# Kernel tuning notes

Hardware: AMD Instinct MI355X
Metric: run time of the kernel (lower is better)

The kernel has to match this reference:

```python
import jax, jax.numpy as jnp
import numpy as np

B, S, D, H = 4, 2048, 1024, 16
DK = D // H

def setup_inputs() -> dict:
    key = jax.random.key(0)
    ks = jax.random.split(key, 9)
    s = 1.0 / np.sqrt(D)
    return {
        "x":  jax.random.normal(ks[0], (B, S, D), dtype=jnp.float32),
        "Wq": jax.random.uniform(ks[1], (D, D), jnp.float32, -s, s),
        "bq": jax.random.uniform(ks[2], (D,), jnp.float32, -s, s),
        "Wk": jax.random.uniform(ks[3], (D, D), jnp.float32, -s, s),
        "bk": jax.random.uniform(ks[4], (D,), jnp.float32, -s, s),
        "Wv": jax.random.uniform(ks[5], (D, D), jnp.float32, -s, s),
        "bv": jax.random.uniform(ks[6], (D,), jnp.float32, -s, s),
        "Wo": jax.random.uniform(ks[7], (D, D), jnp.float32, -s, s),
        "bo": jax.random.uniform(ks[8], (D,), jnp.float32, -s, s),
    }

def reference(x, Wq, bq, Wk, bk, Wv, bv, Wo, bo):
    # Q/K/V projections: [B,S,D] -> [B,H,S,DK]
    def proj(W, b):
        return (x @ W.T + b).reshape(B, S, H, DK).transpose(0, 2, 1, 3)
    Q, K, V = proj(Wq, bq), proj(Wk, bk), proj(Wv, bv)
    scale = 1.0 / np.sqrt(DK).astype(np.float32)
    scores = jnp.einsum('bhqd,bhkd->bhqk', Q, K) * scale  # [B,H,S,S]
    attn = jax.nn.softmax(scores, axis=-1)                 # dropout = identity (eval)
    out = jnp.einsum('bhqk,bhkd->bhqd', attn, V)           # [B,H,S,DK]
    out = out.transpose(0, 2, 1, 3).reshape(B, S, D)
    return out @ Wo.T + bo, attn
```

## Files before the change

### kernel.cpp

```cpp
#include <hip/hip_runtime.h>
#include <hip/hip_bf16.h>

#define Bb 4
#define Ss 2048
#define Dd 1024
#define Hh 16
#define DKk 64

typedef float f32x4 __attribute__((ext_vector_type(4)));
typedef short bf16x8 __attribute__((ext_vector_type(8)));

#define MFMA16(a, b, c) __builtin_amdgcn_mfma_f32_16x16x32_bf16((a), (b), (c), 0, 0, 0)

__device__ __forceinline__ unsigned short f2bf(float f) {
  union { float f; unsigned u; } v;
  v.f = f;
  unsigned r = v.u + 0x7FFFu + ((v.u >> 16) & 1u);
  return (unsigned short)(r >> 16);
}

__device__ __forceinline__ float fast_exp2(float x) {
  float r;
  asm("v_exp_f32 %0, %1" : "=v"(r) : "v"(x));
  return r;
}

__device__ __forceinline__ bf16x8 cvt8(float4 f0, float4 f1) {
  bf16x8 r;
  r[0] = (short)f2bf(f0.x); r[1] = (short)f2bf(f0.y);
  r[2] = (short)f2bf(f0.z); r[3] = (short)f2bf(f0.w);
  r[4] = (short)f2bf(f1.x); r[5] = (short)f2bf(f1.y);
  r[6] = (short)f2bf(f1.z); r[7] = (short)f2bf(f1.w);
  return r;
}

__global__ __launch_bounds__(256) void qkv_proj_kernel(
    const float* __restrict__ X,
    const float* __restrict__ Wq, const float* __restrict__ bq,
    const float* __restrict__ Wk, const float* __restrict__ bk_,
    const float* __restrict__ Wv, const float* __restrict__ bv_,
    unsigned short* __restrict__ qo, unsigned short* __restrict__ ko,
    unsigned short* __restrict__ vo)
{
  __shared__ unsigned short Al[128][72];
  __shared__ unsigned short Bl[128][72];
  const int tid = threadIdx.x;
  const int lane = tid & 63, wid = tid >> 6;
  const int m0 = blockIdx.x * 128;
  const int sel = blockIdx.y >> 3;
  const int n0 = (blockIdx.y & 7) * 128;
  const float* W; const float* bias; unsigned short* out; float prescale;
  if (sel == 0)      { W = Wq; bias = bq;  out = qo; prescale = 0.125f; }
  else if (sel == 1) { W = Wk; bias = bk_; out = ko; prescale = 1.0f;  }
  else               { W = Wv; bias = bv_; out = vo; prescale = 1.0f;  }

  const int wm = (wid >> 1) * 64, wn = (wid & 1) * 64;
  const int lr = lane & 15, lk8 = (lane >> 4) * 8;

  f32x4 acc[4][4] = {};

  for (int k0 = 0; k0 < Dd; k0 += 64) {
#pragma unroll
    for (int it = 0; it < 4; ++it) {
      int idx = it * 256 + tid;
      int row = idx >> 3;
      int ch = (idx & 7) * 8;
      const float* pa = X + (size_t)(m0 + row) * Dd + k0 + ch;
      const float* pb = W + (size_t)(n0 + row) * Dd + k0 + ch;
      float4 a0 = *(const float4*)pa;
      float4 a1 = *(const float4*)(pa + 4);
      float4 b0 = *(const float4*)pb;
      float4 b1 = *(const float4*)(pb + 4);
      *(bf16x8*)&Al[row][ch] = cvt8(a0, a1);
      *(bf16x8*)&Bl[row][ch] = cvt8(b0, b1);
    }
    __syncthreads();
#pragma unroll
    for (int ks = 0; ks < 2; ++ks) {
      const int kk = ks * 32 + lk8;
      bf16x8 av[4], bv[4];
#pragma unroll
      for (int i = 0; i < 4; ++i)
        av[i] = *(const bf16x8*)&Al[wm + i * 16 + lr][kk];
#pragma unroll
      for (int j = 0; j < 4; ++j)
        bv[j] = *(const bf16x8*)&Bl[wn + j * 16 + lr][kk];
#pragma unroll
      for (int i = 0; i < 4; ++i)
#pragma unroll
        for (int j = 0; j < 4; ++j)
          acc[i][j] = MFMA16(av[i], bv[j], acc[i][j]);
    }
    __syncthreads();
  }

  const int rg = (lane >> 4) * 4;
#pragma unroll
  for (int i = 0; i < 4; ++i) {
#pragma unroll
    for (int j = 0; j < 4; ++j) {
      int n = n0 + wn + j * 16 + lr;
      float bvv = bias[n];
      int hh = n >> 6, dk = n & 63;
#pragma unroll
      for (int r = 0; r < 4; ++r) {
        int m = m0 + wm + i * 16 + rg + r;
        int bb = m >> 11, ss = m & (Ss - 1);
        float v = (acc[i][j][r] + bvv) * prescale;
        out[((size_t)(bb * Hh + hh) * Ss + ss) * DKk + dk] = f2bf(v);
      }
    }
  }
}

__global__ __launch_bounds__(256) void attn_kernel(
    const unsigned short* __restrict__ Qw, const unsigned short* __restrict__ Kw,
    const unsigned short* __restrict__ Vw, float* __restrict__ attn,
    unsigned short* __restrict__ OH)
{
  __shared__ unsigned short VT[64][72];
  __shared__ unsigned short Pl[4][32][72];
  const int tid = threadIdx.x, lane = tid & 63, wid = tid >> 6;
  const int bh = blockIdx.y;
  const int q0 = blockIdx.x * 128 + wid * 32;
  const unsigned short* Qh = Qw + (size_t)bh * Ss * DKk;
  const unsigned short* Kh = Kw + (size_t)bh * Ss * DKk;
  const unsigned short* Vh = Vw + (size_t)bh * Ss * DKk;
  const int lr = lane & 15;
  const int lk8 = (lane >> 4) * 8;
  const int rg = (lane >> 4) * 4;
  const float L2E = 1.44269504088896f;

  bf16x8 aq[2][2];
#pragma unroll
  for (int mi = 0; mi < 2; ++mi)
#pragma unroll
    for (int ks = 0; ks < 2; ++ks)
      aq[mi][ks] = *(const bf16x8*)&Qh[(size_t)(q0 + mi * 16 + lr) * DKk + ks * 32 + lk8];

  float lsum[2] = {0.f, 0.f};
  for (int kb = 0; kb < Ss; kb += 64) {
    bf16x8 bk[4][2];
#pragma unroll
    for (int nj = 0; nj < 4; ++nj)
#pragma unroll
      for (int ks = 0; ks < 2; ++ks)
        bk[nj][ks] = *(const bf16x8*)&Kh[(size_t)(kb + nj * 16 + lr) * DKk + ks * 32 + lk8];
#pragma unroll
    for (int mi = 0; mi < 2; ++mi) {
      float acc = 0.f;
#pragma unroll
      for (int nj = 0; nj < 4; ++nj) {
        f32x4 c = {};
        c = MFMA16(bk[nj][0], aq[mi][0], c);
        c = MFMA16(bk[nj][1], aq[mi][1], c);
        acc += fast_exp2(c[0] * L2E) + fast_exp2(c[1] * L2E) +
               fast_exp2(c[2] * L2E) + fast_exp2(c[3] * L2E);
      }
      lsum[mi] += acc;
    }
  }
  float linv[2];
#pragma unroll
  for (int mi = 0; mi < 2; ++mi) {
    float l = lsum[mi];
    l += __shfl_xor(l, 16, 64);
    l += __shfl_xor(l, 32, 64);
    linv[mi] = 1.0f / l;
  }

  f32x4 o[2][4] = {};
  float* attn_bh = attn + (size_t)bh * Ss * Ss;
  for (int kb = 0; kb < Ss; kb += 64) {
    __syncthreads();
    {
      int key = tid >> 2;
      int d0 = (tid & 3) * 16;
      bf16x8 v0 = *(const bf16x8*)&Vh[(size_t)(kb + key) * DKk + d0];
      bf16x8 v1 = *(const bf16x8*)&Vh[(size_t)(kb + key) * DKk + d0 + 8];
#pragma unroll
      for (int i = 0; i < 8; ++i) VT[d0 + i][key] = (unsigned short)v0[i];
#pragma unroll
      for (int i = 0; i < 8; ++i) VT[d0 + 8 + i][key] = (unsigned short)v1[i];
    }
    __syncthreads();

    bf16x8 bk[4][2];
#pragma unroll
    for (int nj = 0; nj < 4; ++nj)
#pragma unroll
      for (int ks = 0; ks < 2; ++ks)
        bk[nj][ks] = *(const bf16x8*)&Kh[(size_t)(kb + nj * 16 + lr) * DKk + ks * 32 + lk8];

#pragma unroll
    for (int mi = 0; mi < 2; ++mi) {
      const int q = q0 + mi * 16 + lr;
      const float li = linv[mi];
      float* arow = attn_bh + (size_t)q * Ss + kb;
#pragma unroll
      for (int nj = 0; nj < 4; ++nj) {
        f32x4 c = {};
        c = MFMA16(bk[nj][0], aq[mi][0], c);
        c = MFMA16(bk[nj][1], aq[mi][1], c);
        float p0 = fast_exp2(c[0] * L2E) * li;
        float p1 = fast_exp2(c[1] * L2E) * li;
        float p2 = fast_exp2(c[2] * L2E) * li;
        float p3 = fast_exp2(c[3] * L2E) * li;
        f32x4 pv4 = {p0, p1, p2, p3};
        __builtin_nontemporal_store(pv4, (f32x4*)(arow + nj * 16 + rg));
        unsigned w0 = (unsigned)f2bf(p0) | ((unsigned)f2bf(p1) << 16);
        unsigned w1 = (unsigned)f2bf(p2) | ((unsigned)f2bf(p3) << 16);
        uint2 w = {w0, w1};
        *(uint2*)&Pl[wid][mi * 16 + lr][nj * 16 + rg] = w;
      }
    }
#pragma unroll
    for (int ks = 0; ks < 2; ++ks) {
      const int kk = ks * 32 + lk8;
      bf16x8 ap[2], bv[4];
#pragma unroll
      for (int mi = 0; mi < 2; ++mi)
        ap[mi] = *(const bf16x8*)&Pl[wid][mi * 16 + lr][kk];
#pragma unroll
      for (int nj = 0; nj < 4; ++nj)
        bv[nj] = *(const bf16x8*)&VT[nj * 16 + lr][kk];
#pragma unroll
      for (int mi = 0; mi < 2; ++mi)
#pragma unroll
        for (int nj = 0; nj < 4; ++nj)
          o[mi][nj] = MFMA16(ap[mi], bv[nj], o[mi][nj]);
    }
  }

  const int b = bh >> 4, h = bh & 15;
#pragma unroll
  for (int mi = 0; mi < 2; ++mi)
#pragma unroll
    for (int nj = 0; nj < 4; ++nj)
#pragma unroll
      for (int r = 0; r < 4; ++r) {
        int q = q0 + mi * 16 + rg + r;
        int d = nj * 16 + lr;
        OH[(((size_t)b * Ss + q) * Hh + h) * DKk + d] = f2bf(o[mi][nj][r]);
      }
}

__global__ __launch_bounds__(256) void oproj_kernel(
    const unsigned short* __restrict__ A, const float* __restrict__ W,
    const float* __restrict__ bias, float* __restrict__ out)
{
  __shared__ unsigned short Al[128][72];
  __shared__ unsigned short Bl[128][72];
  const int tid = threadIdx.x;
  const int lane = tid & 63, wid = tid >> 6;
  const int m0 = blockIdx.x * 128;
  const int n0 = blockIdx.y * 128;
  const int wm = (wid >> 1) * 64, wn = (wid & 1) * 64;
  const int lr = lane & 15, lk8 = (lane >> 4) * 8;

  f32x4 acc[4][4] = {};

  for (int k0 = 0; k0 < Dd; k0 += 64) {
#pragma unroll
    for (int it = 0; it < 4; ++it) {
      int idx = it * 256 + tid;
      int row = idx >> 3;
      int ch = (idx & 7) * 8;
      *(bf16x8*)&Al[row][ch] = *(const bf16x8*)&A[(size_t)(m0 + row) * Dd + k0 + ch];
      const float* pb = W + (size_t)(n0 + row) * Dd + k0 + ch;
      float4 b0 = *(const float4*)pb;
      float4 b1 = *(const float4*)(pb + 4);
      *(bf16x8*)&Bl[row][ch] = cvt8(b0, b1);
    }
    __syncthreads();
#pragma unroll
    for (int ks = 0; ks < 2; ++ks) {
      const int kk = ks * 32 + lk8;
      bf16x8 av[4], bv[4];
#pragma unroll
      for (int i = 0; i < 4; ++i)
        av[i] = *(const bf16x8*)&Al[wm + i * 16 + lr][kk];
#pragma unroll
      for (int j = 0; j < 4; ++j)
        bv[j] = *(const bf16x8*)&Bl[wn + j * 16 + lr][kk];
#pragma unroll
      for (int i = 0; i < 4; ++i)
#pragma unroll
        for (int j = 0; j < 4; ++j)
          acc[i][j] = MFMA16(av[i], bv[j], acc[i][j]);
    }
    __syncthreads();
  }

  const int rg = (lane >> 4) * 4;
#pragma unroll
  for (int i = 0; i < 4; ++i) {
#pragma unroll
    for (int j = 0; j < 4; ++j) {
      int n = n0 + wn + j * 16 + lr;
      float bvv = bias[n];
#pragma unroll
      for (int r = 0; r < 4; ++r) {
        int m = m0 + wm + i * 16 + rg + r;
        out[(size_t)m * Dd + n] = acc[i][j][r] + bvv;
      }
    }
  }
}

extern "C" void kernel_launch(void* const* d_in, const int* in_sizes, int n_in,
                              void* d_out, int out_size, void* d_ws, size_t ws_size,
                              hipStream_t stream) {
  const float* x  = (const float*)d_in[0];
  const float* Wq = (const float*)d_in[1];
  const float* bq = (const float*)d_in[2];
  const float* Wk = (const float*)d_in[3];
  const float* bk = (const float*)d_in[4];
  const float* Wv = (const float*)d_in[5];
  const float* bv = (const float*)d_in[6];
  const float* Wo = (const float*)d_in[7];
  const float* bo = (const float*)d_in[8];

  float* out  = (float*)d_out;
  float* attn = out + (size_t)Bb * Ss * Dd;

  const size_t headElems = (size_t)Bb * Hh * Ss * DKk;
  unsigned short* qws = (unsigned short*)d_ws;
  unsigned short* kws = qws + headElems;
  unsigned short* vws = kws + headElems;
  unsigned short* ohw = vws + headElems;

  dim3 blk(256);
  qkv_proj_kernel<<<dim3(64, 24), blk, 0, stream>>>(x, Wq, bq, Wk, bk, Wv, bv,
                                                    qws, kws, vws);
  attn_kernel<<<dim3(16, 64), blk, 0, stream>>>(qws, kws, vws, attn, ohw);
  oproj_kernel<<<dim3(64, 8), blk, 0, stream>>>(ohw, Wo, bo, out);
}
```

Measured before the change: 620.5 us.

## Pre-cast inputs to bf16, use direct global-to-LDS loads, write V transposed

Adds a cast kernel that converts x and all weight matrices to bf16 once, so the GEMM kernels can stage tiles with global_load_lds instead of per-thread fp32 loads and conversions. The QKV kernel now writes V in a transposed [bh][dk][s] layout, which lets the attention kernel read V fragments straight from global memory and drop the LDS transpose and two barriers per key block. The attention grid is also remapped to a 1D index that groups heads. The cost is an extra launch plus a round trip through global memory for the bf16 copies, and the GEMM LDS tiles lose their padding, which may cause bank conflicts.

```diff
diff --git a/kernel.cpp b/kernel.cpp
--- a/kernel.cpp
+++ b/kernel.cpp
@@ -9,6 +9,7 @@
 
 typedef float f32x4 __attribute__((ext_vector_type(4)));
 typedef short bf16x8 __attribute__((ext_vector_type(8)));
+typedef unsigned short u16x4 __attribute__((ext_vector_type(4)));
 
 #define MFMA16(a, b, c) __builtin_amdgcn_mfma_f32_16x16x32_bf16((a), (b), (c), 0, 0, 0)
 
@@ -34,57 +35,82 @@
   return r;
 }
 
-__global__ __launch_bounds__(256) void qkv_proj_kernel(
-    const float* __restrict__ X,
-    const float* __restrict__ Wq, const float* __restrict__ bq,
-    const float* __restrict__ Wk, const float* __restrict__ bk_,
-    const float* __restrict__ Wv, const float* __restrict__ bv_,
+__global__ __launch_bounds__(256) void cast_all(
+    const float* __restrict__ x,  const float* __restrict__ Wq,
+    const float* __restrict__ Wk, const float* __restrict__ Wv,
+    const float* __restrict__ Wo,
+    unsigned short* __restrict__ xb,  unsigned short* __restrict__ wqb,
+    unsigned short* __restrict__ wkb, unsigned short* __restrict__ wvb,
+    unsigned short* __restrict__ wob)
+{
+  int bid = blockIdx.x;
+  const float* s; unsigned short* d; size_t base8;
+  if (bid < 4096) { s = x; d = xb; base8 = (size_t)bid * 256; }
+  else {
+    int t = bid - 4096; int w = t >> 9; int off = t & 511;
+    s = (w == 0) ? Wq : (w == 1) ? Wk : (w == 2) ? Wv : Wo;
+    d = (w == 0) ? wqb : (w == 1) ? wkb : (w == 2) ? wvb : wob;
+    base8 = (size_t)off * 256;
+  }
+  size_t i8 = base8 + threadIdx.x;
+  const float4* sp = (const float4*)s + 2 * i8;
+  float4 a = sp[0], b = sp[1];
+  *(bf16x8*)(d + i8 * 8) = cvt8(a, b);
+}
+
+__global__ __launch_bounds__(256) void qkv_kernel(
+    const unsigned short* __restrict__ xb,
+    const unsigned short* __restrict__ wqb, const float* __restrict__ bq,
+    const unsigned short* __restrict__ wkb, const float* __restrict__ bk_,
+    const unsigned short* __restrict__ wvb, const float* __restrict__ bv_,
     unsigned short* __restrict__ qo, unsigned short* __restrict__ ko,
-    unsigned short* __restrict__ vo)
+    unsigned short* __restrict__ vto)
 {
-  __shared__ unsigned short Al[128][72];
-  __shared__ unsigned short Bl[128][72];
-  const int tid = threadIdx.x;
-  const int lane = tid & 63, wid = tid >> 6;
+  __shared__ __align__(16) unsigned short Al[128 * 64];
+  __shared__ __align__(16) unsigned short Bl[128 * 64];
+  const int tid = threadIdx.x, lane = tid & 63, wid = tid >> 6;
   const int m0 = blockIdx.x * 128;
   const int sel = blockIdx.y >> 3;
   const int n0 = (blockIdx.y & 7) * 128;
-  const float* W; const float* bias; unsigned short* out; float prescale;
-  if (sel == 0)      { W = Wq; bias = bq;  out = qo; prescale = 0.125f; }
-  else if (sel == 1) { W = Wk; bias = bk_; out = ko; prescale = 1.0f;  }
-  else               { W = Wv; bias = bv_; out = vo; prescale = 1.0f;  }
+  const unsigned short* W; const float* bias;
+  if (sel == 0)      { W = wqb; bias = bq;  }
+  else if (sel == 1) { W = wkb; bias = bk_; }
+  else               { W = wvb; bias = bv_; }
+  const float prescale = (sel == 0) ? 0.125f : 1.0f;
 
   const int wm = (wid >> 1) * 64, wn = (wid & 1) * 64;
   const int lr = lane & 15, lk8 = (lane >> 4) * 8;
 
   f32x4 acc[4][4] = {};
+  const unsigned short* Abase = xb + (size_t)m0 * Dd;
+  const unsigned short* Bbase = W + (size_t)n0 * Dd;
 
   for (int k0 = 0; k0 < Dd; k0 += 64) {
 #pragma unroll
-    for (int it = 0; it < 4; ++it) {
-      int idx = it * 256 + tid;
-      int row = idx >> 3;
-      int ch = (idx & 7) * 8;
-      const float* pa = X + (size_t)(m0 + row) * Dd + k0 + ch;
-      const float* pb = W + (size_t)(n0 + row) * Dd + k0 + ch;
-      float4 a0 = *(const float4*)pa;
-      float4 a1 = *(const float4*)(pa + 4);
-      float4 b0 = *(const float4*)pb;
-      float4 b1 = *(const float4*)(pb + 4);
-      *(bf16x8*)&Al[row][ch] = cvt8(a0, a1);
-      *(bf16x8*)&Bl[row][ch] = cvt8(b0, b1);
+    for (int i = 0; i < 4; ++i) {
+      int qq = (wid * 4 + i) * 64 + lane;
+      int row = qq >> 3, c8 = qq & 7;
+      const unsigned short* ga = Abase + (size_t)row * Dd + k0 + c8 * 8;
+      const unsigned short* gb = Bbase + (size_t)row * Dd + k0 + c8 * 8;
+      __builtin_amdgcn_global_load_lds(
+          (const __attribute__((address_space(1))) unsigned int*)ga,
+          (__attribute__((address_space(3))) unsigned int*)(Al + (wid * 4 + i) * 512),
+          16, 0, 0);
+      __builtin_amdgcn_global_load_lds(
+          (const __attribute__((address_space(1))) unsigned int*)gb,
+          (__attribute__((address_space(3))) unsigned int*)(Bl + (wid * 4 + i) * 512),
+          16, 0, 0);
     }
     __syncthreads();
 #pragma unroll
     for (int ks = 0; ks < 2; ++ks) {
-      const int kk = ks * 32 + lk8;
       bf16x8 av[4], bv[4];
 #pragma unroll
       for (int i = 0; i < 4; ++i)
-        av[i] = *(const bf16x8*)&Al[wm + i * 16 + lr][kk];
+        av[i] = *(const bf16x8*)&Al[(wm + i * 16 + lr) * 64 + ks * 32 + lk8];
 #pragma unroll
       for (int j = 0; j < 4; ++j)
-        bv[j] = *(const bf16x8*)&Bl[wn + j * 16 + lr][kk];
+        bv[j] = *(const bf16x8*)&Bl[(wn + j * 16 + lr) * 64 + ks * 32 + lk8];
 #pragma unroll
       for (int i = 0; i < 4; ++i)
 #pragma unroll
@@ -95,19 +121,37 @@
   }
 
   const int rg = (lane >> 4) * 4;
-#pragma unroll
-  for (int i = 0; i < 4; ++i) {
-#pragma unroll
-    for (int j = 0; j < 4; ++j) {
-      int n = n0 + wn + j * 16 + lr;
-      float bvv = bias[n];
-      int hh = n >> 6, dk = n & 63;
-#pragma unroll
-      for (int r = 0; r < 4; ++r) {
-        int m = m0 + wm + i * 16 + rg + r;
-        int bb = m >> 11, ss = m & (Ss - 1);
-        float v = (acc[i][j][r] + bvv) * prescale;
-        out[((size_t)(bb * Hh + hh) * Ss + ss) * DKk + dk] = f2bf(v);
+  if (sel < 2) {
+    unsigned short* out = (sel == 0) ? qo : ko;
+#pragma unroll
+    for (int i = 0; i < 4; ++i)
+#pragma unroll
+      for (int j = 0; j < 4; ++j) {
+        int n = n0 + wn + j * 16 + lr;
+        float bvv = bias[n];
+        int hh = n >> 6, dk = n & 63;
+#pragma unroll
+        for (int r = 0; r < 4; ++r) {
+          int m = m0 + wm + i * 16 + rg + r;
+          int bb = m >> 11, ss = m & (Ss - 1);
+          float v = (acc[i][j][r] + bvv) * prescale;
+          out[((size_t)(bb * Hh + hh) * Ss + ss) * DKk + dk] = f2bf(v);
+        }
+      }
+  } else {
+#pragma unroll
+    for (int i = 0; i < 4; ++i) {
+      int m_base = m0 + wm + i * 16 + rg;
+      int bb = m_base >> 11, ss0 = m_base & (Ss - 1);
+#pragma unroll
+      for (int j = 0; j < 4; ++j) {
+        int n = n0 + wn + j * 16 + lr;
+        float bvv = bias[n];
+        int hh = n >> 6, dk = n & 63;
+        u16x4 pk;
+#pragma unroll
+        for (int r = 0; r < 4; ++r) pk[r] = f2bf(acc[i][j][r] + bvv);
+        *(u16x4*)&vto[((size_t)(bb * Hh + hh) * DKk + dk) * Ss + ss0] = pk;
       }
     }
   }
@@ -115,17 +159,18 @@
 
 __global__ __launch_bounds__(256) void attn_kernel(
     const unsigned short* __restrict__ Qw, const unsigned short* __restrict__ Kw,
-    const unsigned short* __restrict__ Vw, float* __restrict__ attn,
+    const unsigned short* __restrict__ Vt, float* __restrict__ attn,
     unsigned short* __restrict__ OH)
 {
-  __shared__ unsigned short VT[64][72];
   __shared__ unsigned short Pl[4][32][72];
   const int tid = threadIdx.x, lane = tid & 63, wid = tid >> 6;
-  const int bh = blockIdx.y;
-  const int q0 = blockIdx.x * 128 + wid * 32;
+  const int L = blockIdx.x;
+  const int bh = (L & 7) + 8 * (L >> 7);
+  const int qb = (L >> 3) & 15;
+  const int q0 = qb * 128 + wid * 32;
   const unsigned short* Qh = Qw + (size_t)bh * Ss * DKk;
   const unsigned short* Kh = Kw + (size_t)bh * Ss * DKk;
-  const unsigned short* Vh = Vw + (size_t)bh * Ss * DKk;
+  const unsigned short* Vh = Vt + (size_t)bh * DKk * Ss;
   const int lr = lane & 15;
   const int lk8 = (lane >> 4) * 8;
   const int rg = (lane >> 4) * 4;
@@ -172,25 +217,14 @@
   f32x4 o[2][4] = {};
   float* attn_bh = attn + (size_t)bh * Ss * Ss;
   for (int kb = 0; kb < Ss; kb += 64) {
-    __syncthreads();
-    {
-      int key = tid >> 2;
-      int d0 = (tid & 3) * 16;
-      bf16x8 v0 = *(const bf16x8*)&Vh[(size_t)(kb + key) * DKk + d0];
-      bf16x8 v1 = *(const bf16x8*)&Vh[(size_t)(kb + key) * DKk + d0 + 8];
-#pragma unroll
-      for (int i = 0; i < 8; ++i) VT[d0 + i][key] = (unsigned short)v0[i];
-#pragma unroll
-      for (int i = 0; i < 8; ++i) VT[d0 + 8 + i][key] = (unsigned short)v1[i];
-    }
-    __syncthreads();
-
-    bf16x8 bk[4][2];
+    bf16x8 bk[4][2], bvv[4][2];
 #pragma unroll
     for (int nj = 0; nj < 4; ++nj)
 #pragma unroll
-      for (int ks = 0; ks < 2; ++ks)
+      for (int ks = 0; ks < 2; ++ks) {
         bk[nj][ks] = *(const bf16x8*)&Kh[(size_t)(kb + nj * 16 + lr) * DKk + ks * 32 + lk8];
+        bvv[nj][ks] = *(const bf16x8*)&Vh[(size_t)(nj * 16 + lr) * Ss + kb + ks * 32 + lk8];
+      }
 
 #pragma unroll
     for (int mi = 0; mi < 2; ++mi) {
@@ -217,18 +251,15 @@
 #pragma unroll
     for (int ks = 0; ks < 2; ++ks) {
       const int kk = ks * 32 + lk8;
-      bf16x8 ap[2], bv[4];
+      bf16x8 ap[2];
 #pragma unroll
       for (int mi = 0; mi < 2; ++mi)
         ap[mi] = *(const bf16x8*)&Pl[wid][mi * 16 + lr][kk];
 #pragma unroll
-      for (int nj = 0; nj < 4; ++nj)
-        bv[nj] = *(const bf16x8*)&VT[nj * 16 + lr][kk];
-#pragma unroll
       for (int mi = 0; mi < 2; ++mi)
 #pragma unroll
         for (int nj = 0; nj < 4; ++nj)
-          o[mi][nj] = MFMA16(ap[mi], bv[nj], o[mi][nj]);
+          o[mi][nj] = MFMA16(ap[mi], bvv[nj][ks], o[mi][nj]);
     }
   }
 
@@ -246,43 +277,47 @@
 }
 
 __global__ __launch_bounds__(256) void oproj_kernel(
-    const unsigned short* __restrict__ A, const float* __restrict__ W,
+    const unsigned short* __restrict__ A, const unsigned short* __restrict__ W,
     const float* __restrict__ bias, float* __restrict__ out)
 {
-  __shared__ unsigned short Al[128][72];
-  __shared__ unsigned short Bl[128][72];
-  const int tid = threadIdx.x;
-  const int lane = tid & 63, wid = tid >> 6;
+  __shared__ __align__(16) unsigned short Al[128 * 64];
+  __shared__ __align__(16) unsigned short Bl[128 * 64];
+  const int tid = threadIdx.x, lane = tid & 63, wid = tid >> 6;
   const int m0 = blockIdx.x * 128;
   const int n0 = blockIdx.y * 128;
   const int wm = (wid >> 1) * 64, wn = (wid & 1) * 64;
   const int lr = lane & 15, lk8 = (lane >> 4) * 8;
 
   f32x4 acc[4][4] = {};
+  const unsigned short* Abase = A + (size_t)m0 * Dd;
+  const unsigned short* Bbase = W + (size_t)n0 * Dd;
 
   for (int k0 = 0; k0 < Dd; k0 += 64) {
 #pragma unroll
-    for (int it = 0; it < 4; ++it) {
-      int idx = it * 256 + tid;
-      int row = idx >> 3;
-      int ch = (idx & 7) * 8;
-      *(bf16x8*)&Al[row][ch] = *(const bf16x8*)&A[(size_t)(m0 + row) * Dd + k0 + ch];
-      const float* pb = W + (size_t)(n0 + row) * Dd + k0 + ch;
-      float4 b0 = *(const float4*)pb;
-      float4 b1 = *(const float4*)(pb + 4);
-      *(bf16x8*)&Bl[row][ch] = cvt8(b0, b1);
+    for (int i = 0; i < 4; ++i) {
+      int qq = (wid * 4 + i) * 64 + lane;
+      int row = qq >> 3, c8 = qq & 7;
+      const unsigned short* ga = Abase + (size_t)row * Dd + k0 + c8 * 8;
+      const unsigned short* gb = Bbase + (size_t)row * Dd + k0 + c8 * 8;
+      __builtin_amdgcn_global_load_lds(
+          (const __attribute__((address_space(1))) unsigned int*)ga,
+          (__attribute__((address_space(3))) unsigned int*)(Al + (wid * 4 + i) * 512),
+          16, 0, 0);
+      __builtin_amdgcn_global_load_lds(
+          (const __attribute__((address_space(1))) unsigned int*)gb,
+          (__attribute__((address_space(3))) unsigned int*)(Bl + (wid * 4 + i) * 512),
+          16, 0, 0);
     }
     __syncthreads();
 #pragma unroll
     for (int ks = 0; ks < 2; ++ks) {
-      const int kk = ks * 32 + lk8;
       bf16x8 av[4], bv[4];
 #pragma unroll
       for (int i = 0; i < 4; ++i)
-        av[i] = *(const bf16x8*)&Al[wm + i * 16 + lr][kk];
+        av[i] = *(const bf16x8*)&Al[(wm + i * 16 + lr) * 64 + ks * 32 + lk8];
 #pragma unroll
       for (int j = 0; j < 4; ++j)
-        bv[j] = *(const bf16x8*)&Bl[wn + j * 16 + lr][kk];
+        bv[j] = *(const bf16x8*)&Bl[(wn + j * 16 + lr) * 64 + ks * 32 + lk8];
 #pragma unroll
       for (int i = 0; i < 4; ++i)
 #pragma unroll
@@ -294,7 +329,7 @@
 
   const int rg = (lane >> 4) * 4;
 #pragma unroll
-  for (int i = 0; i < 4; ++i) {
+  for (int i = 0; i < 4; ++i)
 #pragma unroll
     for (int j = 0; j < 4; ++j) {
       int n = n0 + wn + j * 16 + lr;
@@ -305,7 +340,6 @@
         out[(size_t)m * Dd + n] = acc[i][j][r] + bvv;
       }
     }
-  }
 }
 
 extern "C" void kernel_launch(void* const* d_in, const int* in_sizes, int n_in,
@@ -325,14 +359,21 @@
   float* attn = out + (size_t)Bb * Ss * Dd;
 
   const size_t headElems = (size_t)Bb * Hh * Ss * DKk;
-  unsigned short* qws = (unsigned short*)d_ws;
-  unsigned short* kws = qws + headElems;
-  unsigned short* vws = kws + headElems;
-  unsigned short* ohw = vws + headElems;
+  const size_t wElems = (size_t)Dd * Dd;
+  unsigned short* qws  = (unsigned short*)d_ws;
+  unsigned short* kws  = qws + headElems;
+  unsigned short* vtws = kws + headElems;
+  unsigned short* ohw  = vtws + headElems;
+  unsigned short* xb   = ohw + headElems;
+  unsigned short* wqb  = xb + headElems;
+  unsigned short* wkb  = wqb + wElems;
+  unsigned short* wvb  = wkb + wElems;
+  unsigned short* wob  = wvb + wElems;
 
   dim3 blk(256);
-  qkv_proj_kernel<<<dim3(64, 24), blk, 0, stream>>>(x, Wq, bq, Wk, bk, Wv, bv,
-                                                    qws, kws, vws);
-  attn_kernel<<<dim3(16, 64), blk, 0, stream>>>(qws, kws, vws, attn, ohw);
-  oproj_kernel<<<dim3(64, 8), blk, 0, stream>>>(ohw, Wo, bo, out);
-}
+  cast_all<<<dim3(6144), blk, 0, stream>>>(x, Wq, Wk, Wv, Wo, xb, wqb, wkb, wvb, wob);
+  qkv_kernel<<<dim3(64, 24), blk, 0, stream>>>(xb, wqb, bq, wkb, bk, wvb, bv,
+                                               qws, kws, vtws);
+  attn_kernel<<<dim3(1024), blk, 0, stream>>>(qws, kws, vtws, attn, ohw);
+  oproj_kernel<<<dim3(64, 8), blk, 0, stream>>>(ohw, wob, bo, out);
+}
```

Result: faster. 547.1 us (-11.8%).
